# Kernel optimization log

Hardware: AMD Instinct MI355X
Metric: run time of the kernel (lower is better)

Reference implementation:

```python
import jax, jax.numpy as jnp
import numpy as np

B, ENC, C, S, K = 8192, 256, 25, 8192, 25  # batch, encoding_dim, n_clusters, samples, k
EPS = 1e-5


def setup_inputs() -> dict:
    key = jax.random.key(0)
    k1, k2, k3 = jax.random.split(key, 3)
    encodings = jax.random.normal(k1, (B, ENC), dtype=jnp.float32)
    categorical = jax.random.uniform(k2, (B, C), dtype=jnp.float32)
    idxs = jax.random.randint(k3, (S,), 0, B)
    return {"encodings": encodings, "categorical": categorical, "idxs": idxs}


def reference(encodings, categorical, idxs):
    # hard cluster assignment and confidence (argmax / max over components)
    hard_groups = jnp.argmax(categorical, axis=1)            # [B] int
    max_groups = jnp.max(categorical, axis=1)                # [B]

    # per-sample full pairwise Euclidean distances, via GEMM instead of
    # materializing [S, B, ENC] diffs (tf.norm(tensor - query, axis=1))
    q = encodings[idxs]                                      # [S, ENC]
    q2 = jnp.sum(q * q, axis=1)[:, None]                     # [S, 1]
    e2 = jnp.sum(encodings * encodings, axis=1)[None, :]     # [1, B]
    d2 = q2 - 2.0 * (q @ encodings.T) + e2                   # [S, B]
    dists = jnp.sqrt(jnp.maximum(d2, 0.0))                   # [S, B]

    # k-th smallest distance == tf.sort(distances)[k]
    kth = -jax.lax.top_k(-dists, K + 1)[0][:, K]             # [S]
    mask = (dists < kth[:, None]).astype(jnp.float32)        # [S, B], ~K ones/row

    # bincount of cluster labels in each neighbourhood -> Shannon entropy
    onehot = jax.nn.one_hot(hard_groups, C, dtype=jnp.float32)  # [B, C]
    counts = mask @ onehot                                   # [S, C]
    n = jnp.sum(mask, axis=1, keepdims=True)                 # [S, 1] neighbourhood size
    p = counts / n
    purity = -jnp.sum(p * jnp.log(p + EPS), axis=1)          # [S]

    # weight entropy by the confidence of the sampled points
    return purity * max_groups[idxs]                         # [S]
```

## Files before the change

kernel.cpp:

```cpp
#include <hip/hip_runtime.h>
#include <hip/hip_fp16.h>
#include <hip/hip_bf16.h>
#include <math.h>

#define NB   8192
#define NENC 256
#define NC   25
#define NS   8192
#define SEL  26
#define CAP  256
#define EPSA 1.25f
#define ZSIG 2.2f
#define SLOTS 16

typedef __attribute__((ext_vector_type(8))) short short8;
typedef __attribute__((ext_vector_type(4))) float f32x4;

__device__ __forceinline__ void gload_lds16(const void* g, void* l) {
  __builtin_amdgcn_global_load_lds(
      (const __attribute__((address_space(1))) unsigned int*)g,
      (__attribute__((address_space(3))) unsigned int*)l,
      16, 0, 0);
}
__device__ __forceinline__ float h2f(unsigned short u) {
  return __half2float(__ushort_as_half(u));
}

__global__ __launch_bounds__(256) void prep_kernel(
    const float* __restrict__ enc, const float* __restrict__ cat,
    float* __restrict__ e2, float* __restrict__ maxg, int* __restrict__ hard,
    ushort* __restrict__ Bbf, float* __restrict__ msum, float* __restrict__ smoms) {
  int gt = blockIdx.x * 256 + threadIdx.x;
  int w = gt >> 6;
  int lane = gt & 63;

  if (blockIdx.x == 0) {
    if (threadIdx.x < NENC) msum[threadIdx.x] = 0.f;
    if (threadIdx.x < 2) smoms[threadIdx.x] = 0.f;
  }

  float4 v = ((const float4*)(enc + (size_t)w * NENC))[lane];
  ushort4 o;
  __hip_bfloat16 h;
  h = __float2bfloat16(v.x); o.x = *(unsigned short*)&h;
  h = __float2bfloat16(v.y); o.y = *(unsigned short*)&h;
  h = __float2bfloat16(v.z); o.z = *(unsigned short*)&h;
  h = __float2bfloat16(v.w); o.w = *(unsigned short*)&h;
  ((ushort4*)(Bbf + (size_t)w * NENC))[lane] = o;

  float ss = v.x * v.x + v.y * v.y + v.z * v.z + v.w * v.w;
  #pragma unroll
  for (int ofs = 32; ofs; ofs >>= 1) ss += __shfl_down(ss, ofs, 64);

  float mv = -INFINITY;
  int mi = 0;
  if (lane < NC) { mv = cat[(size_t)w * NC + lane]; mi = lane; }
  #pragma unroll
  for (int ofs = 32; ofs; ofs >>= 1) {
    float ov = __shfl_down(mv, ofs, 64);
    int   oi = __shfl_down(mi, ofs, 64);
    if (ov > mv || (ov == mv && oi < mi)) { mv = ov; mi = oi; }
  }
  if (lane == 0) { e2[w] = ss; maxg[w] = mv; hard[w] = mi; }
}

__global__ __launch_bounds__(256) void stats_kernel(
    const float* __restrict__ enc, const float* __restrict__ e2,
    float* __restrict__ msum, float* __restrict__ smoms) {
  __shared__ float red[8];
  const int b = blockIdx.x, t = threadIdx.x, lane = t & 63, wv = t >> 6;
  float part = 0.f;
  #pragma unroll 4
  for (int r = 0; r < 128; ++r) part += enc[(size_t)(b * 128 + r) * NENC + t];
  atomicAdd(&msum[t], part);

  float v = (t < 128) ? e2[b * 128 + t] : 0.f;
  float v2 = v * v;
  #pragma unroll
  for (int o = 32; o; o >>= 1) { v += __shfl_down(v, o, 64); v2 += __shfl_down(v2, o, 64); }
  if (lane == 0) { red[wv] = v; red[4 + wv] = v2; }
  __syncthreads();
  if (t == 0) {
    atomicAdd(&smoms[0], red[0] + red[1] + red[2] + red[3]);
    atomicAdd(&smoms[1], red[4] + red[5] + red[6] + red[7]);
  }
}

__global__ __launch_bounds__(256) void thr_kernel(
    const float* __restrict__ enc, const int* __restrict__ idxs,
    const float* __restrict__ e2, const float* __restrict__ msum,
    const float* __restrict__ smoms, ushort* __restrict__ Abf,
    float* __restrict__ q2, float* __restrict__ thr, float* __restrict__ thr2,
    int* __restrict__ ccount, int* __restrict__ flag) {
  int gt = blockIdx.x * 256 + threadIdx.x;
  if (gt < NS) { ccount[gt] = 0; flag[gt] = 0; }
  int s = gt >> 6, lane = gt & 63;
  int qi = idxs[s];
  float4 v = ((const float4*)(enc + (size_t)qi * NENC))[lane];
  ushort4 o;
  __hip_bfloat16 h;
  h = __float2bfloat16(v.x); o.x = *(unsigned short*)&h;
  h = __float2bfloat16(v.y); o.y = *(unsigned short*)&h;
  h = __float2bfloat16(v.z); o.z = *(unsigned short*)&h;
  h = __float2bfloat16(v.w); o.w = *(unsigned short*)&h;
  ((ushort4*)(Abf + (size_t)s * NENC))[lane] = o;

  float4 mv = ((const float4*)msum)[lane];
  float pm = v.x * mv.x + v.y * mv.y + v.z * mv.z + v.w * mv.w;
  #pragma unroll
  for (int ofs = 32; ofs; ofs >>= 1) pm += __shfl_down(pm, ofs, 64);
  if (lane == 0) {
    float q2v = e2[qi];
    float me2 = smoms[0] * (1.f / NB);
    float ve2 = smoms[1] * (1.f / NB) - me2 * me2;
    float qm  = pm * (1.f / NB);
    float mu  = q2v + me2 - 2.f * qm;
    float sig = sqrtf(fmaxf(ve2 + 4.2f * q2v * (me2 / (float)NENC), 1e-3f));
    float tv  = mu - ZSIG * sig;
    q2[s]  = q2v;
    thr[s] = tv;
    if (tv > 0.f) {
      __half hf = __float2half_rd(tv);
      unsigned short hb = __half_as_ushort(hf);
      float mid = 0.5f * (__half2float(hf) + h2f((unsigned short)(hb + 1)));
      thr2[s] = mid;
    } else {
      thr2[s] = tv;
    }
  }
}

__global__ __launch_bounds__(256, 4) void d2gemm(
    const ushort* __restrict__ Abf, const ushort* __restrict__ Bbf,
    const float* __restrict__ q2, const float* __restrict__ e2,
    const float* __restrict__ thr2, int* __restrict__ ccount,
    unsigned int* __restrict__ cand, int* __restrict__ flag) {
  __shared__ ushort lds[16384];

  const int t = threadIdx.x, lane = t & 63, w = t >> 6;
  int id = blockIdx.x;
  int wg = (id & 7) * 512 + (id >> 3);
  const int bm = wg >> 6, bn = wg & 63;
  const int wm = w >> 1, wn = w & 1;

  f32x4 acc[4][4];
  #pragma unroll
  for (int i = 0; i < 4; ++i)
    #pragma unroll
    for (int j = 0; j < 4; ++j) acc[i][j] = (f32x4){0.f, 0.f, 0.f, 0.f};

  const ushort* Ab = Abf + (size_t)(bm * 128) * NENC;
  const ushort* Bb = Bbf + (size_t)(bn * 128) * NENC;

  for (int kk = 0; kk < NENC; kk += 64) {
    if (kk) __syncthreads();
    #pragma unroll
    for (int u = 0; u < 4; ++u) {
      int flat = u * 256 + t;
      int r = flat >> 3, c = flat & 7;
      gload_lds16(Ab + (size_t)r * NENC + kk + ((c ^ (r & 7)) << 3),
                  (char*)lds + (u * 4 + w) * 1024);
    }
    #pragma unroll
    for (int u = 0; u < 4; ++u) {
      int flat = u * 256 + t;
      int r = flat >> 3, c = flat & 7;
      gload_lds16(Bb + (size_t)r * NENC + kk + ((c ^ (r & 7)) << 3),
                  (char*)lds + 16384 + (u * 4 + w) * 1024);
    }
    __syncthreads();

    #pragma unroll
    for (int kf = 0; kf < 2; ++kf) {
      short8 af[4], bg[4];
      int ch = kf * 4 + (lane >> 4);
      #pragma unroll
      for (int i = 0; i < 4; ++i) {
        int r = wm * 64 + i * 16 + (lane & 15);
        af[i] = *(const short8*)&lds[r * 64 + ((ch ^ (r & 7)) << 3)];
      }
      #pragma unroll
      for (int j = 0; j < 4; ++j) {
        int r = wn * 64 + j * 16 + (lane & 15);
        bg[j] = *(const short8*)&lds[8192 + r * 64 + ((ch ^ (r & 7)) << 3)];
      }
      #pragma unroll
      for (int i = 0; i < 4; ++i)
        #pragma unroll
        for (int j = 0; j < 4; ++j)
          acc[i][j] = __builtin_amdgcn_mfma_f32_16x16x32_bf16(af[i], bg[j], acc[i][j], 0, 0, 0);
    }
  }
  __syncthreads();

  int* lcount = (int*)lds;
  unsigned int* lcand = (unsigned int*)lds + 128;
  if (t < 128) lcount[t] = 0;
  __syncthreads();

  float e2c[4];
  #pragma unroll
  for (int j = 0; j < 4; ++j) e2c[j] = e2[bn * 128 + wn * 64 + j * 16 + (lane & 15)];

  #pragma unroll
  for (int i = 0; i < 4; ++i) {
    int rb = wm * 64 + i * 16 + (lane >> 4) * 4;
    float q2r[4], t2r[4];
    #pragma unroll
    for (int reg = 0; reg < 4; ++reg) {
      q2r[reg] = q2[bm * 128 + rb + reg];
      t2r[reg] = thr2[bm * 128 + rb + reg];
    }
    #pragma unroll
    for (int j = 0; j < 4; ++j) {
      int gcol = bn * 128 + wn * 64 + j * 16 + (lane & 15);
      #pragma unroll
      for (int reg = 0; reg < 4; ++reg) {
        float d2 = fmaf(-2.0f, acc[i][j][reg], q2r[reg]) + e2c[j];
        if (d2 <= t2r[reg]) {
          int lr = rb + reg;
          unsigned short hb = __half_as_ushort(__float2half(fmaxf(d2, 0.f)));
          int slot = atomicAdd(&lcount[lr], 1);
          if (slot < SLOTS)
            lcand[lr * SLOTS + slot] = ((unsigned int)hb << 16) | (unsigned int)gcol;
        }
      }
    }
  }
  __syncthreads();

  if (t < 128) {
    int n = lcount[t];
    int grow = bm * 128 + t;
    if (n > SLOTS) { flag[grow] = 1; n = SLOTS; }
    if (n > 0) {
      int base = atomicAdd(&ccount[grow], n);
      for (int k = 0; k < n; ++k) {
        int p = base + k;
        if (p < CAP) cand[(size_t)grow * CAP + p] = lcand[t * SLOTS + k];
      }
    }
  }
}

__global__ __launch_bounds__(256) void refine_kernel(
    const unsigned int* __restrict__ cand, const int* __restrict__ ccount,
    const float* __restrict__ enc, const float* __restrict__ e2,
    const float* __restrict__ q2, const float* __restrict__ thr,
    const int* __restrict__ hard, const float* __restrict__ maxg,
    const int* __restrict__ idxs, int* __restrict__ flag,
    float* __restrict__ out) {
  __shared__ unsigned int keys[4][CAP];
  __shared__ unsigned int ambi[4][64];
  __shared__ float exd[4][64];
  __shared__ int chist[4][NC];
  __shared__ int acount[4];

  const int t = threadIdx.x, lane = t & 63, wv = t >> 6;
  const int s = blockIdx.x * 4 + wv;
  const int qi = idxs[s];
  const float q2v = q2[s];
  const float tv = thr[s];
  const int cnt = ccount[s];

  if (cnt < SEL || cnt > CAP) {
    if (lane == 0) flag[s] = 1;
    return;
  }
  const int nc = cnt;

  for (int k = lane; k < nc; k += 64) keys[wv][k] = cand[(size_t)s * CAP + k];
  if (lane == 0) acount[wv] = 0;
  if (lane < NC) chist[wv][lane] = 0;

  unsigned int mykth = 0xFFFFFFFFu;
  for (int k = lane; k < nc; k += 64) {
    unsigned int ki = keys[wv][k];
    int r = 0;
    for (int j = 0; j < nc; ++j) r += (keys[wv][j] < ki) ? 1 : 0;
    if (r == SEL - 1) mykth = ki;
  }
  unsigned long long bal = __ballot(mykth != 0xFFFFFFFFu);
  int srcl = __ffsll((unsigned long long)bal) - 1;
  unsigned int kthkey = (unsigned int)__shfl((int)mykth, srcl, 64);
  float kv = h2f((unsigned short)(kthkey >> 16));

  if (kv > tv - 2.f * EPSA) {
    if (lane == 0) flag[s] = 1;
    return;
  }
  const float lo = kv - 2.f * EPSA, hi = kv + 2.f * EPSA;

  int nbl = 0;
  for (int k = lane; k < nc; k += 64) {
    unsigned int ki = keys[wv][k];
    float av = h2f((unsigned short)(ki >> 16));
    int col = (int)(ki & 0x1FFFu);
    if (av < lo) {
      ++nbl;
      atomicAdd(&chist[wv][hard[col]], 1);
    } else if (av <= hi) {
      int sl = atomicAdd(&acount[wv], 1);
      if (sl < 64) ambi[wv][sl] = (unsigned int)col;
    }
  }
  #pragma unroll
  for (int o = 32; o; o >>= 1) nbl += __shfl_down(nbl, o, 64);
  int nbelow = __shfl(nbl, 0, 64);
  int na = acount[wv];
  if (na > 64) {
    if (lane == 0) flag[s] = 1;
    return;
  }

  const int g = lane >> 4, sl = lane & 15;
  float4 qf[4];
  #pragma unroll
  for (int j = 0; j < 4; ++j) qf[j] = ((const float4*)(enc + (size_t)qi * NENC))[sl * 4 + j];
  for (int a0 = g; a0 < na; a0 += 4) {
    int col = (int)ambi[wv][a0];
    const float4* er = (const float4*)(enc + (size_t)col * NENC);
    float p = 0.f;
    #pragma unroll
    for (int j = 0; j < 4; ++j) {
      float4 ev = er[sl * 4 + j];
      p += qf[j].x * ev.x + qf[j].y * ev.y + qf[j].z * ev.z + qf[j].w * ev.w;
    }
    #pragma unroll
    for (int o2 = 1; o2 < 16; o2 <<= 1) p += __shfl_xor(p, o2, 64);
    if (sl == 0) exd[wv][a0] = sqrtf(fmaxf((q2v - 2.0f * p) + e2[col], 0.f));
  }

  int rank1 = SEL - nbelow;
  float myv = (lane < na) ? exd[wv][lane] : 1e30f;
  int rl = 0, re = 0;
  for (int j = 0; j < na; ++j) {
    float ov = exd[wv][j];
    rl += (ov < myv) ? 1 : 0;
    re += (ov == myv) ? 1 : 0;
  }
  float mykv = 1e30f;
  if (lane < na && rl <= rank1 - 1 && rank1 - 1 < rl + re) mykv = myv;
  #pragma unroll
  for (int o = 32; o; o >>= 1) mykv = fminf(mykv, __shfl_down(mykv, o, 64));
  float kthdd = __shfl(mykv, 0, 64);

  int nin = 0;
  for (int k = lane; k < na; k += 64) {
    if (exd[wv][k] < kthdd) {
      ++nin;
      atomicAdd(&chist[wv][hard[(int)ambi[wv][k]]], 1);
    }
  }
  #pragma unroll
  for (int o = 32; o; o >>= 1) nin += __shfl_down(nin, o, 64);

  if (lane == 0) {
    float fn = (float)(nbelow + nin);
    float pur = 0.f;
    for (int c = 0; c < NC; ++c) {
      float p = (float)chist[wv][c] / fn;
      pur -= p * logf(p + 1e-5f);
    }
    out[s] = pur * maxg[qi];
  }
}

__global__ __launch_bounds__(256) void fixup_kernel(
    const float* __restrict__ enc, const float* __restrict__ e2,
    const int* __restrict__ hard, const float* __restrict__ maxg,
    const int* __restrict__ idxs, const int* __restrict__ flag,
    float* __restrict__ out) {
  const int s = blockIdx.x;
  if (!flag[s]) return;

  __shared__ float row[NB];
  __shared__ float qsh[NENC];
  __shared__ int   hist[256];
  __shared__ float wredf[4];
  __shared__ int   wredi[4];
  __shared__ int   binfo[2];
  __shared__ int   chist2[NC];

  const int t = threadIdx.x, lane = t & 63, wv = t >> 6;
  const int qi = idxs[s];
  qsh[t] = enc[(size_t)qi * NENC + t];
  hist[t] = 0;
  if (t < NC) chist2[t] = 0;
  __syncthreads();

  float4 q4 = ((const float4*)qsh)[lane];
  float q2v = e2[qi];
  for (int p = wv; p < NB; p += 4) {
    float4 ev = ((const float4*)(enc + (size_t)p * NENC))[lane];
    float pr = q4.x * ev.x + q4.y * ev.y + q4.z * ev.z + q4.w * ev.w;
    #pragma unroll
    for (int o = 32; o; o >>= 1) pr += __shfl_down(pr, o, 64);
    if (lane == 0) row[p] = sqrtf(fmaxf((q2v - 2.0f * pr) + e2[p], 0.f));
  }
  __syncthreads();

  float lmax = 0.f;
  for (int u = 0; u < 32; ++u) lmax = fmaxf(lmax, row[t + u * 256]);
  #pragma unroll
  for (int o = 32; o; o >>= 1) lmax = fmaxf(lmax, __shfl_down(lmax, o, 64));
  if (lane == 0) wredf[wv] = lmax;
  __syncthreads();
  float smax = fmaxf(fmaxf(wredf[0], wredf[1]), fmaxf(wredf[2], wredf[3]));
  float scale = smax > 0.f ? 256.f / smax : 0.f;

  for (int u = 0; u < 32; ++u) {
    float v = row[t + u * 256];
    int b = (int)(v * scale);
    b = b > 255 ? 255 : b;
    atomicAdd(&hist[b], 1);
  }
  __syncthreads();
  if (t == 0) {
    int cum = 0, j = 0;
    for (; j < 256; ++j) { cum += hist[j]; if (cum >= SEL) break; }
    if (j > 255) j = 255;
    binfo[0] = j;
    binfo[1] = SEL - (cum - hist[j]);
  }
  __syncthreads();
  const int jbin = binfo[0];
  int rank = binfo[1];

  float kth = 0.f, last = -1.f;
  bool first = true;
  for (int iter = 0; iter < 32; ++iter) {
    float lmin = INFINITY;
    for (int u = 0; u < 32; ++u) {
      float v = row[t + u * 256];
      bool elig;
      if (first) {
        int b = (int)(v * scale);
        b = b > 255 ? 255 : b;
        elig = (b >= jbin);
      } else {
        elig = (v > last);
      }
      if (elig) lmin = fminf(lmin, v);
    }
    #pragma unroll
    for (int o = 32; o; o >>= 1) lmin = fminf(lmin, __shfl_down(lmin, o, 64));
    __syncthreads();
    if (lane == 0) wredf[wv] = lmin;
    __syncthreads();
    float m = fminf(fminf(wredf[0], wredf[1]), fminf(wredf[2], wredf[3]));

    int lc = 0;
    for (int u = 0; u < 32; ++u) lc += (row[t + u * 256] == m) ? 1 : 0;
    #pragma unroll
    for (int o = 32; o; o >>= 1) lc += __shfl_down(lc, o, 64);
    __syncthreads();
    if (lane == 0) wredi[wv] = lc;
    __syncthreads();
    int c = wredi[0] + wredi[1] + wredi[2] + wredi[3];

    kth = m;
    if (c >= rank) break;
    rank -= c;
    last = m;
    first = false;
  }

  int ln = 0;
  for (int u = 0; u < 32; ++u) {
    int i = t + u * 256;
    if (row[i] < kth) { atomicAdd(&chist2[hard[i]], 1); ++ln; }
  }
  #pragma unroll
  for (int o = 32; o; o >>= 1) ln += __shfl_down(ln, o, 64);
  __syncthreads();
  if (lane == 0) wredi[wv] = ln;
  __syncthreads();
  if (t == 0) {
    float fn = (float)(wredi[0] + wredi[1] + wredi[2] + wredi[3]);
    float pur = 0.f;
    for (int c = 0; c < NC; ++c) {
      float p = (float)chist2[c] / fn;
      pur -= p * logf(p + 1e-5f);
    }
    out[s] = pur * maxg[qi];
  }
}

extern "C" void kernel_launch(void* const* d_in, const int* in_sizes, int n_in,
                              void* d_out, int out_size, void* d_ws, size_t ws_size,
                              hipStream_t stream) {
  const float* enc = (const float*)d_in[0];
  const float* cat = (const float*)d_in[1];
  const int* idxs = (const int*)d_in[2];
  float* out = (float*)d_out;

  char* ws = (char*)d_ws;
  float* e2    = (float*)ws;
  float* maxg  = e2 + NB;
  float* q2    = maxg + NB;
  float* thr   = q2 + NS;
  float* thr2  = thr + NS;
  float* msum  = thr2 + NS;
  float* smoms = msum + NENC;
  int*   hard   = (int*)(smoms + 2);
  int*   ccount = hard + NB;
  int*   flag   = ccount + NS;
  unsigned int* cand = (unsigned int*)(flag + NS);
  ushort* Abf = (ushort*)(cand + (size_t)NS * CAP);
  ushort* Bbf = Abf + (size_t)NS * NENC;

  prep_kernel<<<dim3(NB / 4), dim3(256), 0, stream>>>(enc, cat, e2, maxg, hard, Bbf,
                                                      msum, smoms);
  stats_kernel<<<dim3(64), dim3(256), 0, stream>>>(enc, e2, msum, smoms);
  thr_kernel<<<dim3(NS / 4), dim3(256), 0, stream>>>(enc, idxs, e2, msum, smoms, Abf,
                                                     q2, thr, thr2, ccount, flag);
  d2gemm<<<dim3(4096), dim3(256), 0, stream>>>(Abf, Bbf, q2, e2, thr2, ccount, cand, flag);
  refine_kernel<<<dim3(NS / 4), dim3(256), 0, stream>>>(cand, ccount, enc, e2, q2, thr,
                                                        hard, maxg, idxs, flag, out);
  fixup_kernel<<<dim3(NS), dim3(256), 0, stream>>>(enc, e2, hard, maxg, idxs, flag, out);
}
```

Baseline: 168.2 us.

## Fuse stats into prep, drop mean term, merge refine and fixup kernels

Folds the e2 moment accumulation into prep_kernel and removes stats_kernel. The threshold estimate no longer uses the per-query dot product with the column mean, which assumes the encodings are roughly zero-mean. refine and fixup are merged into one kernel, where flagged rows are recomputed in-block by the same block, replacing a separate 8192-block launch. It also raises d2gemm's occupancy hint from 4 to 5. The risk is that the changed threshold raises the rate of flagged fallbacks, and those fallbacks now run serially inside a block.

```diff
diff --git a/kernel.cpp b/kernel.cpp
--- a/kernel.cpp
+++ b/kernel.cpp
@@ -29,15 +29,14 @@
 __global__ __launch_bounds__(256) void prep_kernel(
     const float* __restrict__ enc, const float* __restrict__ cat,
     float* __restrict__ e2, float* __restrict__ maxg, int* __restrict__ hard,
-    ushort* __restrict__ Bbf, float* __restrict__ msum, float* __restrict__ smoms) {
+    ushort* __restrict__ Bbf, float* __restrict__ smoms,
+    int* __restrict__ ccount, int* __restrict__ flag) {
+  __shared__ float pr[8];
   int gt = blockIdx.x * 256 + threadIdx.x;
   int w = gt >> 6;
   int lane = gt & 63;
 
-  if (blockIdx.x == 0) {
-    if (threadIdx.x < NENC) msum[threadIdx.x] = 0.f;
-    if (threadIdx.x < 2) smoms[threadIdx.x] = 0.f;
-  }
+  if (gt < NS) { ccount[gt] = 0; flag[gt] = 0; }
 
   float4 v = ((const float4*)(enc + (size_t)w * NENC))[lane];
   ushort4 o;
@@ -61,39 +60,24 @@
     int   oi = __shfl_down(mi, ofs, 64);
     if (ov > mv || (ov == mv && oi < mi)) { mv = ov; mi = oi; }
   }
-  if (lane == 0) { e2[w] = ss; maxg[w] = mv; hard[w] = mi; }
-}
-
-__global__ __launch_bounds__(256) void stats_kernel(
-    const float* __restrict__ enc, const float* __restrict__ e2,
-    float* __restrict__ msum, float* __restrict__ smoms) {
-  __shared__ float red[8];
-  const int b = blockIdx.x, t = threadIdx.x, lane = t & 63, wv = t >> 6;
-  float part = 0.f;
-  #pragma unroll 4
-  for (int r = 0; r < 128; ++r) part += enc[(size_t)(b * 128 + r) * NENC + t];
-  atomicAdd(&msum[t], part);
-
-  float v = (t < 128) ? e2[b * 128 + t] : 0.f;
-  float v2 = v * v;
-  #pragma unroll
-  for (int o = 32; o; o >>= 1) { v += __shfl_down(v, o, 64); v2 += __shfl_down(v2, o, 64); }
-  if (lane == 0) { red[wv] = v; red[4 + wv] = v2; }
+  int wv = threadIdx.x >> 6;
+  if (lane == 0) {
+    e2[w] = ss; maxg[w] = mv; hard[w] = mi;
+    pr[wv] = ss; pr[4 + wv] = ss * ss;
+  }
   __syncthreads();
-  if (t == 0) {
-    atomicAdd(&smoms[0], red[0] + red[1] + red[2] + red[3]);
-    atomicAdd(&smoms[1], red[4] + red[5] + red[6] + red[7]);
+  if (threadIdx.x == 0) {
+    atomicAdd(&smoms[0], pr[0] + pr[1] + pr[2] + pr[3]);
+    atomicAdd(&smoms[1], pr[4] + pr[5] + pr[6] + pr[7]);
   }
 }
 
 __global__ __launch_bounds__(256) void thr_kernel(
     const float* __restrict__ enc, const int* __restrict__ idxs,
-    const float* __restrict__ e2, const float* __restrict__ msum,
-    const float* __restrict__ smoms, ushort* __restrict__ Abf,
-    float* __restrict__ q2, float* __restrict__ thr, float* __restrict__ thr2,
-    int* __restrict__ ccount, int* __restrict__ flag) {
+    const float* __restrict__ e2, const float* __restrict__ smoms,
+    ushort* __restrict__ Abf, float* __restrict__ q2,
+    float* __restrict__ thr, float* __restrict__ thr2) {
   int gt = blockIdx.x * 256 + threadIdx.x;
-  if (gt < NS) { ccount[gt] = 0; flag[gt] = 0; }
   int s = gt >> 6, lane = gt & 63;
   int qi = idxs[s];
   float4 v = ((const float4*)(enc + (size_t)qi * NENC))[lane];
@@ -105,16 +89,11 @@
   h = __float2bfloat16(v.w); o.w = *(unsigned short*)&h;
   ((ushort4*)(Abf + (size_t)s * NENC))[lane] = o;
 
-  float4 mv = ((const float4*)msum)[lane];
-  float pm = v.x * mv.x + v.y * mv.y + v.z * mv.z + v.w * mv.w;
-  #pragma unroll
-  for (int ofs = 32; ofs; ofs >>= 1) pm += __shfl_down(pm, ofs, 64);
   if (lane == 0) {
     float q2v = e2[qi];
     float me2 = smoms[0] * (1.f / NB);
     float ve2 = smoms[1] * (1.f / NB) - me2 * me2;
-    float qm  = pm * (1.f / NB);
-    float mu  = q2v + me2 - 2.f * qm;
+    float mu  = q2v + me2;
     float sig = sqrtf(fmaxf(ve2 + 4.2f * q2v * (me2 / (float)NENC), 1e-3f));
     float tv  = mu - ZSIG * sig;
     q2[s]  = q2v;
@@ -130,7 +109,7 @@
   }
 }
 
-__global__ __launch_bounds__(256, 4) void d2gemm(
+__global__ __launch_bounds__(256, 5) void d2gemm(
     const ushort* __restrict__ Abf, const ushort* __restrict__ Bbf,
     const float* __restrict__ q2, const float* __restrict__ e2,
     const float* __restrict__ thr2, int* __restrict__ ccount,
@@ -243,247 +222,252 @@
   }
 }
 
-__global__ __launch_bounds__(256) void refine_kernel(
+__global__ __launch_bounds__(256) void refine_fix(
     const unsigned int* __restrict__ cand, const int* __restrict__ ccount,
     const float* __restrict__ enc, const float* __restrict__ e2,
     const float* __restrict__ q2, const float* __restrict__ thr,
     const int* __restrict__ hard, const float* __restrict__ maxg,
-    const int* __restrict__ idxs, int* __restrict__ flag,
+    const int* __restrict__ idxs, const int* __restrict__ flag,
     float* __restrict__ out) {
-  __shared__ unsigned int keys[4][CAP];
-  __shared__ unsigned int ambi[4][64];
-  __shared__ float exd[4][64];
-  __shared__ int chist[4][NC];
-  __shared__ int acount[4];
+  __shared__ char smem[35072];
+  unsigned int* keys = (unsigned int*)smem;
+  unsigned int* ambi = keys + 4 * CAP;
+  float* exd  = (float*)(ambi + 4 * 64);
+  int* chist  = (int*)(exd + 4 * 64);
+  int* acount = chist + 4 * NC;
+  int* lflag  = acount + 4;
+  float* rowb = (float*)smem;
+  float* qsh  = (float*)(smem + 32768);
+  int*  hist  = (int*)(smem + 33792);
+  float* wredf = (float*)(smem + 34816);
+  int*  wredi  = (int*)(smem + 34832);
+  int*  binfo  = (int*)(smem + 34848);
+  int*  chist2 = (int*)(smem + 34856);
 
   const int t = threadIdx.x, lane = t & 63, wv = t >> 6;
-  const int s = blockIdx.x * 4 + wv;
+  const int s0 = blockIdx.x * 4;
+  const int s = s0 + wv;
   const int qi = idxs[s];
   const float q2v = q2[s];
   const float tv = thr[s];
   const int cnt = ccount[s];
 
-  if (cnt < SEL || cnt > CAP) {
-    if (lane == 0) flag[s] = 1;
-    return;
-  }
-  const int nc = cnt;
-
-  for (int k = lane; k < nc; k += 64) keys[wv][k] = cand[(size_t)s * CAP + k];
-  if (lane == 0) acount[wv] = 0;
-  if (lane < NC) chist[wv][lane] = 0;
-
-  unsigned int mykth = 0xFFFFFFFFu;
-  for (int k = lane; k < nc; k += 64) {
-    unsigned int ki = keys[wv][k];
-    int r = 0;
-    for (int j = 0; j < nc; ++j) r += (keys[wv][j] < ki) ? 1 : 0;
-    if (r == SEL - 1) mykth = ki;
-  }
-  unsigned long long bal = __ballot(mykth != 0xFFFFFFFFu);
-  int srcl = __ffsll((unsigned long long)bal) - 1;
-  unsigned int kthkey = (unsigned int)__shfl((int)mykth, srcl, 64);
-  float kv = h2f((unsigned short)(kthkey >> 16));
-
-  if (kv > tv - 2.f * EPSA) {
-    if (lane == 0) flag[s] = 1;
-    return;
-  }
-  const float lo = kv - 2.f * EPSA, hi = kv + 2.f * EPSA;
-
-  int nbl = 0;
-  for (int k = lane; k < nc; k += 64) {
-    unsigned int ki = keys[wv][k];
-    float av = h2f((unsigned short)(ki >> 16));
-    int col = (int)(ki & 0x1FFFu);
-    if (av < lo) {
-      ++nbl;
-      atomicAdd(&chist[wv][hard[col]], 1);
-    } else if (av <= hi) {
-      int sl = atomicAdd(&acount[wv], 1);
-      if (sl < 64) ambi[wv][sl] = (unsigned int)col;
-    }
-  }
-  #pragma unroll
-  for (int o = 32; o; o >>= 1) nbl += __shfl_down(nbl, o, 64);
-  int nbelow = __shfl(nbl, 0, 64);
-  int na = acount[wv];
-  if (na > 64) {
-    if (lane == 0) flag[s] = 1;
-    return;
-  }
-
-  const int g = lane >> 4, sl = lane & 15;
-  float4 qf[4];
-  #pragma unroll
-  for (int j = 0; j < 4; ++j) qf[j] = ((const float4*)(enc + (size_t)qi * NENC))[sl * 4 + j];
-  for (int a0 = g; a0 < na; a0 += 4) {
-    int col = (int)ambi[wv][a0];
-    const float4* er = (const float4*)(enc + (size_t)col * NENC);
-    float p = 0.f;
-    #pragma unroll
-    for (int j = 0; j < 4; ++j) {
-      float4 ev = er[sl * 4 + j];
-      p += qf[j].x * ev.x + qf[j].y * ev.y + qf[j].z * ev.z + qf[j].w * ev.w;
-    }
-    #pragma unroll
-    for (int o2 = 1; o2 < 16; o2 <<= 1) p += __shfl_xor(p, o2, 64);
-    if (sl == 0) exd[wv][a0] = sqrtf(fmaxf((q2v - 2.0f * p) + e2[col], 0.f));
-  }
-
-  int rank1 = SEL - nbelow;
-  float myv = (lane < na) ? exd[wv][lane] : 1e30f;
-  int rl = 0, re = 0;
-  for (int j = 0; j < na; ++j) {
-    float ov = exd[wv][j];
-    rl += (ov < myv) ? 1 : 0;
-    re += (ov == myv) ? 1 : 0;
-  }
-  float mykv = 1e30f;
-  if (lane < na && rl <= rank1 - 1 && rank1 - 1 < rl + re) mykv = myv;
-  #pragma unroll
-  for (int o = 32; o; o >>= 1) mykv = fminf(mykv, __shfl_down(mykv, o, 64));
-  float kthdd = __shfl(mykv, 0, 64);
-
-  int nin = 0;
-  for (int k = lane; k < na; k += 64) {
-    if (exd[wv][k] < kthdd) {
-      ++nin;
-      atomicAdd(&chist[wv][hard[(int)ambi[wv][k]]], 1);
-    }
-  }
-  #pragma unroll
-  for (int o = 32; o; o >>= 1) nin += __shfl_down(nin, o, 64);
-
-  if (lane == 0) {
-    float fn = (float)(nbelow + nin);
-    float pur = 0.f;
-    for (int c = 0; c < NC; ++c) {
-      float p = (float)chist[wv][c] / fn;
-      pur -= p * logf(p + 1e-5f);
-    }
-    out[s] = pur * maxg[qi];
-  }
-}
-
-__global__ __launch_bounds__(256) void fixup_kernel(
-    const float* __restrict__ enc, const float* __restrict__ e2,
-    const int* __restrict__ hard, const float* __restrict__ maxg,
-    const int* __restrict__ idxs, const int* __restrict__ flag,
-    float* __restrict__ out) {
-  const int s = blockIdx.x;
-  if (!flag[s]) return;
-
-  __shared__ float row[NB];
-  __shared__ float qsh[NENC];
-  __shared__ int   hist[256];
-  __shared__ float wredf[4];
-  __shared__ int   wredi[4];
-  __shared__ int   binfo[2];
-  __shared__ int   chist2[NC];
-
-  const int t = threadIdx.x, lane = t & 63, wv = t >> 6;
-  const int qi = idxs[s];
-  qsh[t] = enc[(size_t)qi * NENC + t];
-  hist[t] = 0;
-  if (t < NC) chist2[t] = 0;
+  if (lane == 0) { lflag[wv] = flag[s]; acount[wv] = 0; }
+  if (lane < NC) chist[wv * NC + lane] = 0;
+
+  bool bad = (flag[s] != 0) || (cnt < SEL) || (cnt > CAP);
+  const int nc = bad ? 0 : cnt;
+
+  if (!bad) {
+    unsigned int* kw = keys + wv * CAP;
+    for (int k = lane; k < nc; k += 64) kw[k] = cand[(size_t)s * CAP + k];
+
+    unsigned int mykth = 0xFFFFFFFFu;
+    for (int k = lane; k < nc; k += 64) {
+      unsigned int ki = kw[k];
+      int r = 0;
+      for (int j = 0; j < nc; ++j) r += (kw[j] < ki) ? 1 : 0;
+      if (r == SEL - 1) mykth = ki;
+    }
+    unsigned long long bal = __ballot(mykth != 0xFFFFFFFFu);
+    int srcl = __ffsll((unsigned long long)bal) - 1;
+    unsigned int kthkey = (unsigned int)__shfl((int)mykth, srcl, 64);
+    float kv = h2f((unsigned short)(kthkey >> 16));
+
+    if (kv > tv - 2.f * EPSA) {
+      bad = true;
+      if (lane == 0) lflag[wv] = 1;
+    } else {
+      const float lo = kv - 2.f * EPSA, hi = kv + 2.f * EPSA;
+      int nbl = 0;
+      for (int k = lane; k < nc; k += 64) {
+        unsigned int ki = kw[k];
+        float av = h2f((unsigned short)(ki >> 16));
+        int col = (int)(ki & 0x1FFFu);
+        if (av < lo) {
+          ++nbl;
+          atomicAdd(&chist[wv * NC + hard[col]], 1);
+        } else if (av <= hi) {
+          int sl = atomicAdd(&acount[wv], 1);
+          if (sl < 64) ambi[wv * 64 + sl] = (unsigned int)col;
+        }
+      }
+      #pragma unroll
+      for (int o = 32; o; o >>= 1) nbl += __shfl_down(nbl, o, 64);
+      int nbelow = __shfl(nbl, 0, 64);
+      int na = acount[wv];
+      if (na > 64) {
+        bad = true;
+        if (lane == 0) lflag[wv] = 1;
+      } else {
+        const int g = lane >> 4, sl = lane & 15;
+        float4 qf[4];
+        #pragma unroll
+        for (int j = 0; j < 4; ++j)
+          qf[j] = ((const float4*)(enc + (size_t)qi * NENC))[sl * 4 + j];
+        for (int a0 = g; a0 < na; a0 += 4) {
+          int col = (int)ambi[wv * 64 + a0];
+          const float4* er = (const float4*)(enc + (size_t)col * NENC);
+          float p = 0.f;
+          #pragma unroll
+          for (int j = 0; j < 4; ++j) {
+            float4 ev = er[sl * 4 + j];
+            p += qf[j].x * ev.x + qf[j].y * ev.y + qf[j].z * ev.z + qf[j].w * ev.w;
+          }
+          #pragma unroll
+          for (int o2 = 1; o2 < 16; o2 <<= 1) p += __shfl_xor(p, o2, 64);
+          if (sl == 0) exd[wv * 64 + a0] = sqrtf(fmaxf((q2v - 2.0f * p) + e2[col], 0.f));
+        }
+
+        int rank1 = SEL - nbelow;
+        float myv = (lane < na) ? exd[wv * 64 + lane] : 1e30f;
+        int rl = 0, re = 0;
+        for (int j = 0; j < na; ++j) {
+          float ov = exd[wv * 64 + j];
+          rl += (ov < myv) ? 1 : 0;
+          re += (ov == myv) ? 1 : 0;
+        }
+        float mykv = 1e30f;
+        if (lane < na && rl <= rank1 - 1 && rank1 - 1 < rl + re) mykv = myv;
+        #pragma unroll
+        for (int o = 32; o; o >>= 1) mykv = fminf(mykv, __shfl_down(mykv, o, 64));
+        float kthdd = __shfl(mykv, 0, 64);
+
+        int nin = 0;
+        for (int k = lane; k < na; k += 64) {
+          if (exd[wv * 64 + k] < kthdd) {
+            ++nin;
+            atomicAdd(&chist[wv * NC + hard[(int)ambi[wv * 64 + k]]], 1);
+          }
+        }
+        #pragma unroll
+        for (int o = 32; o; o >>= 1) nin += __shfl_down(nin, o, 64);
+
+        if (lane == 0) {
+          float fn = (float)(nbelow + nin);
+          float pur = 0.f;
+          for (int c = 0; c < NC; ++c) {
+            float p = (float)chist[wv * NC + c] / fn;
+            pur -= p * logf(p + 1e-5f);
+          }
+          out[s] = pur * maxg[qi];
+        }
+      }
+    }
+  }
+
   __syncthreads();
-
-  float4 q4 = ((const float4*)qsh)[lane];
-  float q2v = e2[qi];
-  for (int p = wv; p < NB; p += 4) {
-    float4 ev = ((const float4*)(enc + (size_t)p * NENC))[lane];
-    float pr = q4.x * ev.x + q4.y * ev.y + q4.z * ev.z + q4.w * ev.w;
-    #pragma unroll
-    for (int o = 32; o; o >>= 1) pr += __shfl_down(pr, o, 64);
-    if (lane == 0) row[p] = sqrtf(fmaxf((q2v - 2.0f * pr) + e2[p], 0.f));
-  }
+  int f0 = lflag[0], f1 = lflag[1], f2 = lflag[2], f3 = lflag[3];
   __syncthreads();
-
-  float lmax = 0.f;
-  for (int u = 0; u < 32; ++u) lmax = fmaxf(lmax, row[t + u * 256]);
-  #pragma unroll
-  for (int o = 32; o; o >>= 1) lmax = fmaxf(lmax, __shfl_down(lmax, o, 64));
-  if (lane == 0) wredf[wv] = lmax;
-  __syncthreads();
-  float smax = fmaxf(fmaxf(wredf[0], wredf[1]), fmaxf(wredf[2], wredf[3]));
-  float scale = smax > 0.f ? 256.f / smax : 0.f;
-
-  for (int u = 0; u < 32; ++u) {
-    float v = row[t + u * 256];
-    int b = (int)(v * scale);
-    b = b > 255 ? 255 : b;
-    atomicAdd(&hist[b], 1);
-  }
-  __syncthreads();
-  if (t == 0) {
-    int cum = 0, j = 0;
-    for (; j < 256; ++j) { cum += hist[j]; if (cum >= SEL) break; }
-    if (j > 255) j = 255;
-    binfo[0] = j;
-    binfo[1] = SEL - (cum - hist[j]);
-  }
-  __syncthreads();
-  const int jbin = binfo[0];
-  int rank = binfo[1];
-
-  float kth = 0.f, last = -1.f;
-  bool first = true;
-  for (int iter = 0; iter < 32; ++iter) {
-    float lmin = INFINITY;
+  if (!(f0 | f1 | f2 | f3)) return;
+
+  for (int r = 0; r < 4; ++r) {
+    int fr = (r == 0) ? f0 : (r == 1) ? f1 : (r == 2) ? f2 : f3;
+    if (!fr) continue;
+    const int sf = s0 + r;
+    const int qif = idxs[sf];
+    qsh[t] = enc[(size_t)qif * NENC + t];
+    hist[t] = 0;
+    if (t < NC) chist2[t] = 0;
+    __syncthreads();
+
+    float4 q4 = ((const float4*)qsh)[lane];
+    float q2f = e2[qif];
+    for (int p = wv; p < NB; p += 4) {
+      float4 ev = ((const float4*)(enc + (size_t)p * NENC))[lane];
+      float pr = q4.x * ev.x + q4.y * ev.y + q4.z * ev.z + q4.w * ev.w;
+      #pragma unroll
+      for (int o = 32; o; o >>= 1) pr += __shfl_down(pr, o, 64);
+      if (lane == 0) rowb[p] = sqrtf(fmaxf((q2f - 2.0f * pr) + e2[p], 0.f));
+    }
+    __syncthreads();
+
+    float lmax = 0.f;
+    for (int u = 0; u < 32; ++u) lmax = fmaxf(lmax, rowb[t + u * 256]);
+    #pragma unroll
+    for (int o = 32; o; o >>= 1) lmax = fmaxf(lmax, __shfl_down(lmax, o, 64));
+    if (lane == 0) wredf[wv] = lmax;
+    __syncthreads();
+    float smax = fmaxf(fmaxf(wredf[0], wredf[1]), fmaxf(wredf[2], wredf[3]));
+    float scale = smax > 0.f ? 256.f / smax : 0.f;
+
     for (int u = 0; u < 32; ++u) {
-      float v = row[t + u * 256];
-      bool elig;
-      if (first) {
-        int b = (int)(v * scale);
-        b = b > 255 ? 255 : b;
-        elig = (b >= jbin);
-      } else {
-        elig = (v > last);
-      }
-      if (elig) lmin = fminf(lmin, v);
-    }
-    #pragma unroll
-    for (int o = 32; o; o >>= 1) lmin = fminf(lmin, __shfl_down(lmin, o, 64));
-    __syncthreads();
-    if (lane == 0) wredf[wv] = lmin;
-    __syncthreads();
-    float m = fminf(fminf(wredf[0], wredf[1]), fminf(wredf[2], wredf[3]));
-
-    int lc = 0;
-    for (int u = 0; u < 32; ++u) lc += (row[t + u * 256] == m) ? 1 : 0;
-    #pragma unroll
-    for (int o = 32; o; o >>= 1) lc += __shfl_down(lc, o, 64);
-    __syncthreads();
-    if (lane == 0) wredi[wv] = lc;
-    __syncthreads();
-    int c = wredi[0] + wredi[1] + wredi[2] + wredi[3];
-
-    kth = m;
-    if (c >= rank) break;
-    rank -= c;
-    last = m;
-    first = false;
-  }
-
-  int ln = 0;
-  for (int u = 0; u < 32; ++u) {
-    int i = t + u * 256;
-    if (row[i] < kth) { atomicAdd(&chist2[hard[i]], 1); ++ln; }
-  }
-  #pragma unroll
-  for (int o = 32; o; o >>= 1) ln += __shfl_down(ln, o, 64);
-  __syncthreads();
-  if (lane == 0) wredi[wv] = ln;
-  __syncthreads();
-  if (t == 0) {
-    float fn = (float)(wredi[0] + wredi[1] + wredi[2] + wredi[3]);
-    float pur = 0.f;
-    for (int c = 0; c < NC; ++c) {
-      float p = (float)chist2[c] / fn;
-      pur -= p * logf(p + 1e-5f);
-    }
-    out[s] = pur * maxg[qi];
+      float v = rowb[t + u * 256];
+      int b = (int)(v * scale);
+      b = b > 255 ? 255 : b;
+      atomicAdd(&hist[b], 1);
+    }
+    __syncthreads();
+    if (t == 0) {
+      int cum = 0, j = 0;
+      for (; j < 256; ++j) { cum += hist[j]; if (cum >= SEL) break; }
+      if (j > 255) j = 255;
+      binfo[0] = j;
+      binfo[1] = SEL - (cum - hist[j]);
+    }
+    __syncthreads();
+    const int jbin = binfo[0];
+    int rank = binfo[1];
+
+    float kth = 0.f, last = -1.f;
+    bool first = true;
+    for (int iter = 0; iter < 32; ++iter) {
+      float lmin = INFINITY;
+      for (int u = 0; u < 32; ++u) {
+        float v = rowb[t + u * 256];
+        bool elig;
+        if (first) {
+          int b = (int)(v * scale);
+          b = b > 255 ? 255 : b;
+          elig = (b >= jbin);
+        } else {
+          elig = (v > last);
+        }
+        if (elig) lmin = fminf(lmin, v);
+      }
+      #pragma unroll
+      for (int o = 32; o; o >>= 1) lmin = fminf(lmin, __shfl_down(lmin, o, 64));
+      __syncthreads();
+      if (lane == 0) wredf[wv] = lmin;
+      __syncthreads();
+      float m = fminf(fminf(wredf[0], wredf[1]), fminf(wredf[2], wredf[3]));
+
+      int lc = 0;
+      for (int u = 0; u < 32; ++u) lc += (rowb[t + u * 256] == m) ? 1 : 0;
+      #pragma unroll
+      for (int o = 32; o; o >>= 1) lc += __shfl_down(lc, o, 64);
+      __syncthreads();
+      if (lane == 0) wredi[wv] = lc;
+      __syncthreads();
+      int c = wredi[0] + wredi[1] + wredi[2] + wredi[3];
+
+      kth = m;
+      if (c >= rank) break;
+      rank -= c;
+      last = m;
+      first = false;
+    }
+
+    int ln = 0;
+    for (int u = 0; u < 32; ++u) {
+      int i = t + u * 256;
+      if (rowb[i] < kth) { atomicAdd(&chist2[hard[i]], 1); ++ln; }
+    }
+    #pragma unroll
+    for (int o = 32; o; o >>= 1) ln += __shfl_down(ln, o, 64);
+    __syncthreads();
+    if (lane == 0) wredi[wv] = ln;
+    __syncthreads();
+    if (t == 0) {
+      float fn = (float)(wredi[0] + wredi[1] + wredi[2] + wredi[3]);
+      float pur = 0.f;
+      for (int c = 0; c < NC; ++c) {
+        float p = (float)chist2[c] / fn;
+        pur -= p * logf(p + 1e-5f);
+      }
+      out[sf] = pur * maxg[qif];
+    }
+    __syncthreads();
   }
 }
 
@@ -501,8 +485,7 @@
   float* q2    = maxg + NB;
   float* thr   = q2 + NS;
   float* thr2  = thr + NS;
-  float* msum  = thr2 + NS;
-  float* smoms = msum + NENC;
+  float* smoms = thr2 + NS;
   int*   hard   = (int*)(smoms + 2);
   int*   ccount = hard + NB;
   int*   flag   = ccount + NS;
@@ -510,13 +493,12 @@
   ushort* Abf = (ushort*)(cand + (size_t)NS * CAP);
   ushort* Bbf = Abf + (size_t)NS * NENC;
 
+  hipMemsetAsync(smoms, 0, 2 * sizeof(float), stream);
   prep_kernel<<<dim3(NB / 4), dim3(256), 0, stream>>>(enc, cat, e2, maxg, hard, Bbf,
-                                                      msum, smoms);
-  stats_kernel<<<dim3(64), dim3(256), 0, stream>>>(enc, e2, msum, smoms);
-  thr_kernel<<<dim3(NS / 4), dim3(256), 0, stream>>>(enc, idxs, e2, msum, smoms, Abf,
-                                                     q2, thr, thr2, ccount, flag);
+                                                      smoms, ccount, flag);
+  thr_kernel<<<dim3(NS / 4), dim3(256), 0, stream>>>(enc, idxs, e2, smoms, Abf,
+                                                     q2, thr, thr2);
   d2gemm<<<dim3(4096), dim3(256), 0, stream>>>(Abf, Bbf, q2, e2, thr2, ccount, cand, flag);
-  refine_kernel<<<dim3(NS / 4), dim3(256), 0, stream>>>(cand, ccount, enc, e2, q2, thr,
-                                                        hard, maxg, idxs, flag, out);
-  fixup_kernel<<<dim3(NS), dim3(256), 0, stream>>>(enc, e2, hard, maxg, idxs, flag, out);
-}
+  refine_fix<<<dim3(NS / 4), dim3(256), 0, stream>>>(cand, ccount, enc, e2, q2, thr,
+                                                     hard, maxg, idxs, flag, out);
+}
```

Measured after the change: 300.0 us. 78.3% more time.
